# Kernel optimization log

Measured on AMD Instinct MI355X. Metric: run time of the kernel, lower is better.

## Reference

```python
import jax, jax.numpy as jnp
import numpy as np

B = 4096
D = 1024
WEIGHT = 1.0
EPS = 1e-7  # Keras K.epsilon()


def setup_inputs() -> dict:
    key = jax.random.key(0)
    k1, k2 = jax.random.split(key)
    return {
        "left": jax.random.normal(k1, (B, D), dtype=jnp.float32),
        "right": jax.random.normal(k2, (B, D), dtype=jnp.float32),
        "temperature": jnp.zeros((1,), dtype=jnp.float32),
    }


def _l2_normalize(x):
    # matches l2_norm: sqrt(max(sum(x^2), eps))
    sq = jnp.sum(jnp.square(x), axis=-1, keepdims=True)
    return x / jnp.sqrt(jnp.maximum(sq, EPS))


def reference(left, right, temperature):
    ln = _l2_normalize(left)   # [B, D]
    rn = _l2_normalize(right)  # [B, D]
    scale = jnp.exp(temperature)  # (1,) broadcasts
    logits_left = jnp.einsum("bd,cd->bc", ln, rn) * scale   # [B, B]
    logits_right = logits_left.T                             # rn @ ln.T * scale
    prob_left = jax.nn.softmax(logits_left, axis=-1)
    prob_right = jax.nn.softmax(logits_right, axis=-1)
    # NOTE: the original calls CCE(prob, labels), i.e. y_true=prob, y_pred=eye.
    # Keras clips y_pred to [eps, 1-eps]; loss = -sum(y_true * log(clip(y_pred))).
    labels = jnp.eye(B, dtype=jnp.float32)
    log_clipped = jnp.log(jnp.clip(labels, EPS, 1.0 - EPS))  # diag: log(1-eps), off: log(eps)
    loss_left = -jnp.sum(prob_left * log_clipped)
    loss_right = -jnp.sum(prob_right * log_clipped)
    loss = (loss_left + loss_right) / 2.0 / B
    return WEIGHT * loss
```

## Files before the change

kernel.cpp:

```cpp
#include <hip/hip_runtime.h>
#include <hip/hip_bf16.h>

#define Bn 4096
#define Dk 1024
#define EPSF 1e-7f

typedef float f32x16 __attribute__((ext_vector_type(16)));
typedef int i32x4 __attribute__((ext_vector_type(4)));
typedef int i32x8 __attribute__((ext_vector_type(8)));

__device__ __forceinline__ void async_copy16(const void* g, void* l) {
    __builtin_amdgcn_global_load_lds((__attribute__((address_space(1))) void*)(uintptr_t)g,
                                     (__attribute__((address_space(3))) void*)l, 16, 0, 0);
}

__global__ __launch_bounds__(256)
void nrm_kernel(const float4* __restrict__ left, const float4* __restrict__ right,
                unsigned char* __restrict__ lnb8, unsigned char* __restrict__ rnb8,
                float* __restrict__ diag, float* __restrict__ rowsum,
                float* __restrict__ colsum)
{
    const int row = blockIdx.x;
    const int t = threadIdx.x;
    const int idx = row * (Dk / 4) + t;
    const float4 l = left[idx];
    const float4 r = right[idx];
    float sl = l.x * l.x + l.y * l.y + l.z * l.z + l.w * l.w;
    float sr = r.x * r.x + r.y * r.y + r.z * r.z + r.w * r.w;
    float slr = l.x * r.x + l.y * r.y + l.z * r.z + l.w * r.w;
    #pragma unroll
    for (int off = 1; off < 64; off <<= 1) {
        sl += __shfl_xor(sl, off);
        sr += __shfl_xor(sr, off);
        slr += __shfl_xor(slr, off);
    }
    __shared__ float red[3][4];
    const int wave = t >> 6, lane = t & 63;
    if (lane == 0) { red[0][wave] = sl; red[1][wave] = sr; red[2][wave] = slr; }
    __syncthreads();
    sl = red[0][0] + red[0][1] + red[0][2] + red[0][3];
    sr = red[1][0] + red[1][1] + red[1][2] + red[1][3];
    const float invl = 1.0f / sqrtf(fmaxf(sl, EPSF));
    const float invr = 1.0f / sqrtf(fmaxf(sr, EPSF));
    const float sL = 8.0f * invl;
    const float sR = 8.0f * invr;
    int pkL = __builtin_amdgcn_cvt_pk_fp8_f32(l.x * sL, l.y * sL, 0, false);
    pkL = __builtin_amdgcn_cvt_pk_fp8_f32(l.z * sL, l.w * sL, pkL, true);
    int pkR = __builtin_amdgcn_cvt_pk_fp8_f32(r.x * sR, r.y * sR, 0, false);
    pkR = __builtin_amdgcn_cvt_pk_fp8_f32(r.z * sR, r.w * sR, pkR, true);
    const int dst = row * Dk + 4 * t;
    *(unsigned*)(lnb8 + dst) = (unsigned)pkL;
    *(unsigned*)(rnb8 + dst) = (unsigned)pkR;
    if (t == 0) {
        const float d = red[2][0] + red[2][1] + red[2][2] + red[2][3];
        diag[row] = d * invl * invr;
        rowsum[row] = 0.f;
        colsum[row] = 0.f;
    }
}

__global__ __launch_bounds__(256, 2)
void gemm_sm_kernel(const unsigned char* __restrict__ lnb8,
                    const unsigned char* __restrict__ rnb8,
                    const float* __restrict__ temp,
                    float* __restrict__ rowsum, float* __restrict__ colsum)
{
    __shared__ __align__(16) unsigned char As[2][128 * 64];
    __shared__ __align__(16) unsigned char Bs[2][256 * 64];

    const int tid = threadIdx.x;
    const int wave = tid >> 6;
    const int lane = tid & 63;
    const int bm0 = blockIdx.y * 128;
    const int bn0 = blockIdx.x * 256;

    const int srow = lane >> 2;
    const int sj = lane & 3;
    int goffA[2], lofsA[2];
    #pragma unroll
    for (int i = 0; i < 2; ++i) {
        const int rloc = wave * 32 + i * 16 + srow;
        goffA[i] = rloc * Dk + 16 * (sj ^ ((rloc >> 1) & 3));
        lofsA[i] = (wave * 32 + i * 16) * 64;
    }
    int goffB[4], lofsB[4];
    #pragma unroll
    for (int i = 0; i < 4; ++i) {
        const int rloc = wave * 64 + i * 16 + srow;
        goffB[i] = rloc * Dk + 16 * (sj ^ ((rloc >> 1) & 3));
        lofsB[i] = (wave * 64 + i * 16) * 64;
    }
    const unsigned char* baseA = lnb8 + (size_t)bm0 * Dk;
    const unsigned char* baseB = rnb8 + (size_t)bn0 * Dk;

    const int wm = (wave & 1) * 64;
    const int wn = (wave >> 1) * 128;
    const int r32 = lane & 31;
    const int h = lane >> 5;
    int aoff[2][2], boff[4][2];
    #pragma unroll
    for (int mi = 0; mi < 2; ++mi) {
        const int row = wm + mi * 32 + r32;
        const int key = (row >> 1) & 3;
        aoff[mi][0] = row * 64 + 16 * ((2 * h) ^ key);
        aoff[mi][1] = row * 64 + 16 * ((2 * h + 1) ^ key);
    }
    #pragma unroll
    for (int ni = 0; ni < 4; ++ni) {
        const int row = wn + ni * 32 + r32;
        const int key = (row >> 1) & 3;
        boff[ni][0] = row * 64 + 16 * ((2 * h) ^ key);
        boff[ni][1] = row * 64 + 16 * ((2 * h + 1) ^ key);
    }

    f32x16 acc[2][4];
    #pragma unroll
    for (int mi = 0; mi < 2; ++mi)
        #pragma unroll
        for (int ni = 0; ni < 4; ++ni)
            #pragma unroll
            for (int r = 0; r < 16; ++r)
                acc[mi][ni][r] = 0.f;

    #pragma unroll
    for (int i = 0; i < 2; ++i) async_copy16(baseA + goffA[i], &As[0][lofsA[i]]);
    #pragma unroll
    for (int i = 0; i < 4; ++i) async_copy16(baseB + goffB[i], &Bs[0][lofsB[i]]);

    #pragma unroll 2
    for (int it = 0; it < 16; ++it) {
        const int cur = it & 1;
        const int nxt = cur ^ 1;
        const int knext = ((it + 1) & 15) * 64;
        #pragma unroll
        for (int i = 0; i < 2; ++i) async_copy16(baseA + goffA[i] + knext, &As[nxt][lofsA[i]]);
        #pragma unroll
        for (int i = 0; i < 4; ++i) async_copy16(baseB + goffB[i] + knext, &Bs[nxt][lofsB[i]]);
        asm volatile("s_waitcnt vmcnt(6)\n\ts_barrier" ::: "memory");
        i32x8 af[2], bf[4];
        #pragma unroll
        for (int mi = 0; mi < 2; ++mi) {
            const i32x4 lo = *(const i32x4*)(&As[cur][aoff[mi][0]]);
            const i32x4 hi = *(const i32x4*)(&As[cur][aoff[mi][1]]);
            af[mi] = __builtin_shufflevector(lo, hi, 0, 1, 2, 3, 4, 5, 6, 7);
        }
        #pragma unroll
        for (int ni = 0; ni < 4; ++ni) {
            const i32x4 lo = *(const i32x4*)(&Bs[cur][boff[ni][0]]);
            const i32x4 hi = *(const i32x4*)(&Bs[cur][boff[ni][1]]);
            bf[ni] = __builtin_shufflevector(lo, hi, 0, 1, 2, 3, 4, 5, 6, 7);
        }
        #pragma unroll
        for (int mi = 0; mi < 2; ++mi)
            #pragma unroll
            for (int ni = 0; ni < 4; ++ni)
                acc[mi][ni] = __builtin_amdgcn_mfma_scale_f32_32x32x64_f8f6f4(
                    af[mi], bf[ni], acc[mi][ni],
                    0, 0,
                    0, 0x7f7f7f7f,
                    0, 0x7f7f7f7f);
        asm volatile("s_barrier" ::: "memory");
    }

    const float scale = __expf(temp[0]);
    const float dq = 0.015625f * scale;
    #pragma unroll
    for (int mi = 0; mi < 2; ++mi)
        #pragma unroll
        for (int ni = 0; ni < 4; ++ni)
            #pragma unroll
            for (int r = 0; r < 16; ++r)
                acc[mi][ni][r] = __expf(dq * acc[mi][ni][r] - scale);

    #pragma unroll
    for (int mi = 0; mi < 2; ++mi) {
        #pragma unroll
        for (int r = 0; r < 16; ++r) {
            float v = acc[mi][0][r] + acc[mi][1][r] + acc[mi][2][r] + acc[mi][3][r];
            v += __shfl_xor(v, 1);
            v += __shfl_xor(v, 2);
            v += __shfl_xor(v, 4);
            v += __shfl_xor(v, 8);
            v += __shfl_xor(v, 16);
            if (r32 == 0)
                atomicAdd(&rowsum[bm0 + wm + mi * 32 + (r & 3) + 8 * (r >> 2) + 4 * h], v);
        }
    }
    #pragma unroll
    for (int ni = 0; ni < 4; ++ni) {
        float v = 0.f;
        #pragma unroll
        for (int mi = 0; mi < 2; ++mi)
            #pragma unroll
            for (int r = 0; r < 16; ++r)
                v += acc[mi][ni][r];
        v += __shfl_xor(v, 32);
        if (h == 0)
            atomicAdd(&colsum[bn0 + wn + ni * 32 + r32], v);
    }
}

__global__ __launch_bounds__(256)
void loss_kernel(const float* __restrict__ diag, const float* __restrict__ rowsum,
                 const float* __restrict__ colsum, const float* __restrict__ temp,
                 float* __restrict__ out)
{
    const int t = threadIdx.x;
    const float scale = __expf(temp[0]);
    float dL = 0.f, dR = 0.f;
    for (int i = t; i < Bn; i += 256) {
        const float e = __expf(scale * (diag[i] - 1.0f));
        dL += e * __builtin_amdgcn_rcpf(rowsum[i]);
        dR += e * __builtin_amdgcn_rcpf(colsum[i]);
    }
    #pragma unroll
    for (int off = 1; off < 64; off <<= 1) {
        dL += __shfl_xor(dL, off);
        dR += __shfl_xor(dR, off);
    }
    __shared__ float rd[2][4];
    const int wave = t >> 6, lane = t & 63;
    if (lane == 0) { rd[0][wave] = dL; rd[1][wave] = dR; }
    __syncthreads();
    if (t == 0) {
        dL = rd[0][0] + rd[0][1] + rd[0][2] + rd[0][3];
        dR = rd[1][0] + rd[1][1] + rd[1][2] + rd[1][3];
        const float logeps = logf(EPSF);
        const float log1m = logf(1.0f - EPSF);
        const float lossL = -(dL * log1m + ((float)Bn - dL) * logeps);
        const float lossR = -(dR * log1m + ((float)Bn - dR) * logeps);
        out[0] = (lossL + lossR) * 0.5f / (float)Bn;
    }
}

extern "C" void kernel_launch(void* const* d_in, const int* in_sizes, int n_in,
                              void* d_out, int out_size, void* d_ws, size_t ws_size,
                              hipStream_t stream) {
    (void)in_sizes; (void)n_in; (void)out_size; (void)ws_size;
    const float* left = (const float*)d_in[0];
    const float* right = (const float*)d_in[1];
    const float* temp = (const float*)d_in[2];

    char* ws = (char*)d_ws;
    unsigned char* lnb8 = (unsigned char*)ws;
    unsigned char* rnb8 = (unsigned char*)(ws + (size_t)Bn * Dk);
    float* diag = (float*)(ws + 2 * (size_t)Bn * Dk);
    float* rowsum = diag + Bn;
    float* colsum = rowsum + Bn;

    nrm_kernel<<<Bn, 256, 0, stream>>>((const float4*)left, (const float4*)right,
                                       lnb8, rnb8, diag, rowsum, colsum);
    dim3 g2(Bn / 256, Bn / 128);
    gemm_sm_kernel<<<g2, 256, 0, stream>>>(lnb8, rnb8, temp, rowsum, colsum);
    loss_kernel<<<1, 256, 0, stream>>>(diag, rowsum, colsum, temp, (float*)d_out);
}
```

Measured before the change: 106.8 us.

## Load B operand straight from global into registers, bypassing LDS

After: 129.4 us. 21.2% more time.

```diff
diff --git a/kernel.cpp b/kernel.cpp
--- a/kernel.cpp
+++ b/kernel.cpp
@@ -66,7 +66,6 @@
                     float* __restrict__ rowsum, float* __restrict__ colsum)
 {
     __shared__ __align__(16) unsigned char As[2][128 * 64];
-    __shared__ __align__(16) unsigned char Bs[2][256 * 64];
 
     const int tid = threadIdx.x;
     const int wave = tid >> 6;
@@ -83,21 +82,13 @@
         goffA[i] = rloc * Dk + 16 * (sj ^ ((rloc >> 1) & 3));
         lofsA[i] = (wave * 32 + i * 16) * 64;
     }
-    int goffB[4], lofsB[4];
-    #pragma unroll
-    for (int i = 0; i < 4; ++i) {
-        const int rloc = wave * 64 + i * 16 + srow;
-        goffB[i] = rloc * Dk + 16 * (sj ^ ((rloc >> 1) & 3));
-        lofsB[i] = (wave * 64 + i * 16) * 64;
-    }
     const unsigned char* baseA = lnb8 + (size_t)bm0 * Dk;
-    const unsigned char* baseB = rnb8 + (size_t)bn0 * Dk;
 
     const int wm = (wave & 1) * 64;
     const int wn = (wave >> 1) * 128;
     const int r32 = lane & 31;
     const int h = lane >> 5;
-    int aoff[2][2], boff[4][2];
+    int aoff[2][2];
     #pragma unroll
     for (int mi = 0; mi < 2; ++mi) {
         const int row = wm + mi * 32 + r32;
@@ -105,13 +96,10 @@
         aoff[mi][0] = row * 64 + 16 * ((2 * h) ^ key);
         aoff[mi][1] = row * 64 + 16 * ((2 * h + 1) ^ key);
     }
-    #pragma unroll
-    for (int ni = 0; ni < 4; ++ni) {
-        const int row = wn + ni * 32 + r32;
-        const int key = (row >> 1) & 3;
-        boff[ni][0] = row * 64 + 16 * ((2 * h) ^ key);
-        boff[ni][1] = row * 64 + 16 * ((2 * h + 1) ^ key);
-    }
+    const unsigned char* bbase[4];
+    #pragma unroll
+    for (int ni = 0; ni < 4; ++ni)
+        bbase[ni] = rnb8 + (size_t)(bn0 + wn + ni * 32 + r32) * Dk + 32 * h;
 
     f32x16 acc[2][4];
     #pragma unroll
@@ -124,8 +112,13 @@
 
     #pragma unroll
     for (int i = 0; i < 2; ++i) async_copy16(baseA + goffA[i], &As[0][lofsA[i]]);
-    #pragma unroll
-    for (int i = 0; i < 4; ++i) async_copy16(baseB + goffB[i], &Bs[0][lofsB[i]]);
+    i32x8 bf[4];
+    #pragma unroll
+    for (int ni = 0; ni < 4; ++ni) {
+        const i32x4 lo = *(const i32x4*)(bbase[ni]);
+        const i32x4 hi = *(const i32x4*)(bbase[ni] + 16);
+        bf[ni] = __builtin_shufflevector(lo, hi, 0, 1, 2, 3, 4, 5, 6, 7);
+    }
 
     #pragma unroll 2
     for (int it = 0; it < 16; ++it) {
@@ -134,21 +127,20 @@
         const int knext = ((it + 1) & 15) * 64;
         #pragma unroll
         for (int i = 0; i < 2; ++i) async_copy16(baseA + goffA[i] + knext, &As[nxt][lofsA[i]]);
-        #pragma unroll
-        for (int i = 0; i < 4; ++i) async_copy16(baseB + goffB[i] + knext, &Bs[nxt][lofsB[i]]);
-        asm volatile("s_waitcnt vmcnt(6)\n\ts_barrier" ::: "memory");
-        i32x8 af[2], bf[4];
+        asm volatile("s_waitcnt vmcnt(10)\n\ts_barrier" ::: "memory");
+        i32x8 af[2];
         #pragma unroll
         for (int mi = 0; mi < 2; ++mi) {
             const i32x4 lo = *(const i32x4*)(&As[cur][aoff[mi][0]]);
             const i32x4 hi = *(const i32x4*)(&As[cur][aoff[mi][1]]);
             af[mi] = __builtin_shufflevector(lo, hi, 0, 1, 2, 3, 4, 5, 6, 7);
         }
+        i32x8 nbf[4];
         #pragma unroll
         for (int ni = 0; ni < 4; ++ni) {
-            const i32x4 lo = *(const i32x4*)(&Bs[cur][boff[ni][0]]);
-            const i32x4 hi = *(const i32x4*)(&Bs[cur][boff[ni][1]]);
-            bf[ni] = __builtin_shufflevector(lo, hi, 0, 1, 2, 3, 4, 5, 6, 7);
+            const i32x4 lo = *(const i32x4*)(bbase[ni] + knext);
+            const i32x4 hi = *(const i32x4*)(bbase[ni] + knext + 16);
+            nbf[ni] = __builtin_shufflevector(lo, hi, 0, 1, 2, 3, 4, 5, 6, 7);
         }
         #pragma unroll
         for (int mi = 0; mi < 2; ++mi)
@@ -160,6 +152,8 @@
                     0, 0x7f7f7f7f,
                     0, 0x7f7f7f7f);
         asm volatile("s_barrier" ::: "memory");
+        #pragma unroll
+        for (int ni = 0; ni < 4; ++ni) bf[ni] = nbf[ni];
     }
 
     const float scale = __expf(temp[0]);
```
